# Performance work log

Hardware: AMD Instinct MI355X
Metric: run time of the kernel (lower is better)

Reference implementation:

```python
import jax, jax.numpy as jnp
import numpy as np
import math

C = 512          # in_planes
H = 8            # num_heads
D = C // H       # head_dim = 64
EPS = 1e-12      # torch F.normalize eps


def _l2norm(x):
    # F.normalize(x, dim=-1): x / max(||x||_2, eps)
    n = jnp.sqrt(jnp.sum(x * x, axis=-1, keepdims=True))
    return x / jnp.maximum(n, EPS)


def setup_inputs() -> dict:
    key = jax.random.key(0)
    ks = jax.random.split(key, 8)
    q = jax.random.normal(ks[0], (8, 8, 256, C), dtype=jnp.float32)
    kv = jax.random.normal(ks[1], (8, 8, 512, C), dtype=jnp.float32)
    s = 0.02
    Wq = jax.random.normal(ks[2], (C, C), dtype=jnp.float32) * s
    bq = jax.random.normal(ks[3], (C,), dtype=jnp.float32) * s
    Wkv = jax.random.normal(ks[4], (2 * C, C), dtype=jnp.float32) * s
    bkv = jax.random.normal(ks[5], (2 * C,), dtype=jnp.float32) * s
    Wm = jax.random.normal(ks[6], (C, C), dtype=jnp.float32) * s
    bm = jax.random.normal(ks[7], (C,), dtype=jnp.float32) * s
    return {"q": q, "kv": kv, "Wq": Wq, "bq": bq, "Wkv": Wkv, "bkv": bkv, "Wm": Wm, "bm": bm}


def reference(q, kv, Wq, bq, Wkv, bkv, Wm, bm):
    b, t, lq, c = q.shape
    lk = kv.shape[2]
    shortcut = q

    # Q projection -> (b,t,h,lq,d), L2-normalized over d
    qh = (q @ Wq.T + bq).reshape(b, t, lq, H, D)
    qh = _l2norm(jnp.moveaxis(qh, 3, 2))  # (b,t,h,lq,d)

    # KV projection -> (b,t,2h,lk,d); first H heads = k, last H = v
    kvh = (kv @ Wkv.T + bkv).reshape(b, t, lk, 2 * H, D)
    kvh = jnp.moveaxis(kvh, 3, 2)          # (b,t,2h,lk,d)
    kh = _l2norm(kvh[:, :, :H])            # (b,t,h,lk,d)
    vh = _l2norm(kvh[:, :, H:])            # (b,t,h,lk,d)

    # cosine attention
    att = jnp.einsum('bthqd,bthkd->bthqk', qh, kh) / math.sqrt(D)
    att = jax.nn.softmax(att, axis=-1)
    x = jnp.einsum('bthqk,bthkd->bthqd', att, vh)  # (b,t,h,lq,d)

    # merge heads, output projection, residual
    x = jnp.moveaxis(x, 2, 3).reshape(b, t, lq, c)
    return x @ Wm.T + bm + shortcut
```

## Files before the change

kernel.cpp:

```cpp
#include <hip/hip_runtime.h>
#include <hip/hip_bf16.h>

using bf = __bf16;
typedef __attribute__((ext_vector_type(8))) __bf16 bf16x8;
typedef __attribute__((ext_vector_type(4))) float f32x4;

#define MFMA(a, b, c) __builtin_amdgcn_mfma_f32_16x16x32_bf16((a), (b), (c), 0, 0, 0)
#define GLL16(g, s)                                                         \
    __builtin_amdgcn_global_load_lds(                                       \
        (const __attribute__((address_space(1))) void*)(g),                 \
        (__attribute__((address_space(3))) void*)(s), 16, 0, 0)

__global__ __launch_bounds__(256) void cvt8(const float* __restrict__ s,
                                            bf* __restrict__ d, int n8)
{
    const int i = blockIdx.x * 256 + threadIdx.x;
    if (i >= n8) return;
    const f32x4 a = ((const f32x4*)s)[2 * i];
    const f32x4 b = ((const f32x4*)s)[2 * i + 1];
    bf16x8 r;
#pragma unroll
    for (int k = 0; k < 4; ++k) { r[k] = (bf)a[k]; r[4 + k] = (bf)b[k]; }
    ((bf16x8*)d)[i] = r;
}

template <int EPI>
__global__ __launch_bounds__(256) void gemm128(
    const bf* __restrict__ A, const bf* __restrict__ W,
    const float* __restrict__ bias, const float* __restrict__ res,
    void* __restrict__ Cout, int M, int N, int K)
{
    __shared__ __attribute__((aligned(16))) bf As[128 * 32];
    __shared__ __attribute__((aligned(16))) bf Bs[128 * 32];

    const int lane = threadIdx.x & 63;
    const int wave = threadIdx.x >> 6;
    const int lm = lane & 15;
    const int quad = lane >> 4;
    const int row0 = blockIdx.x * 128, col0 = blockIdx.y * 128;
    const int wrow = (wave >> 1) * 64, wcol = (wave & 1) * 64;

    const int sr = lane >> 2;
    const int sc = (lane & 3) * 8;
    const bf* Ag = A + (size_t)(row0 + wave * 32 + sr) * K + sc;
    const bf* Wg = W + (size_t)(col0 + wave * 32 + sr) * K + sc;
    bf* AsW = As + wave * 1024;
    bf* BsW = Bs + wave * 1024;

    f32x4 acc[4][4] = {};

    for (int k0 = 0; k0 < K; k0 += 32) {
        GLL16(Ag + k0, AsW);
        GLL16(Ag + (size_t)16 * K + k0, AsW + 512);
        GLL16(Wg + k0, BsW);
        GLL16(Wg + (size_t)16 * K + k0, BsW + 512);
        __syncthreads();

        bf16x8 a[4], b[4];
#pragma unroll
        for (int i = 0; i < 4; ++i)
            a[i] = *(const bf16x8*)(As + (wrow + i * 16 + lm) * 32 + quad * 8);
#pragma unroll
        for (int j = 0; j < 4; ++j)
            b[j] = *(const bf16x8*)(Bs + (wcol + j * 16 + lm) * 32 + quad * 8);
#pragma unroll
        for (int i = 0; i < 4; ++i)
#pragma unroll
            for (int j = 0; j < 4; ++j)
                acc[i][j] = MFMA(a[i], b[j], acc[i][j]);
        __syncthreads();
    }

    float bv[4];
#pragma unroll
    for (int j = 0; j < 4; ++j) bv[j] = bias[col0 + wcol + j * 16 + lm];

    if (EPI == 0) {
        bf* C = (bf*)Cout;
#pragma unroll
        for (int i = 0; i < 4; ++i) {
#pragma unroll
            for (int r = 0; r < 4; ++r) {
                float v[4];
                float ss = 0.f;
#pragma unroll
                for (int j = 0; j < 4; ++j) {
                    const float x = acc[i][j][r] + bv[j];
                    v[j] = x;
                    ss += x * x;
                }
                ss += __shfl_xor(ss, 1, 64);
                ss += __shfl_xor(ss, 2, 64);
                ss += __shfl_xor(ss, 4, 64);
                ss += __shfl_xor(ss, 8, 64);
                const float inv = 1.0f / fmaxf(sqrtf(ss), 1e-12f);
                const int row = row0 + wrow + i * 16 + quad * 4 + r;
#pragma unroll
                for (int j = 0; j < 4; ++j)
                    C[(size_t)row * N + col0 + wcol + j * 16 + lm] = (bf)(v[j] * inv);
            }
        }
    } else {
        float* C = (float*)Cout;
#pragma unroll
        for (int i = 0; i < 4; ++i) {
#pragma unroll
            for (int r = 0; r < 4; ++r) {
                const int row = row0 + wrow + i * 16 + quad * 4 + r;
#pragma unroll
                for (int j = 0; j < 4; ++j) {
                    const size_t idx = (size_t)row * N + col0 + wcol + j * 16 + lm;
                    C[idx] = acc[i][j][r] + bv[j] + res[idx];
                }
            }
        }
    }
}

__global__ __launch_bounds__(256) void attn(
    const bf* __restrict__ qn, const bf* __restrict__ kvn, bf* __restrict__ X)
{
    __shared__ __attribute__((aligned(16))) bf kS[512 * 72];
    __shared__ __attribute__((aligned(16))) bf vT[64 * 520];
    __shared__ __attribute__((aligned(16))) bf Ps[4][16 * 40];

    const int bt = blockIdx.x >> 3;
    const int h = blockIdx.x & 7;
    const int tid = threadIdx.x;
    const int lane = tid & 63;
    const int wave = tid >> 6;
    const int lm = lane & 15;
    const int quad = lane >> 4;

    const bf* qh = qn + (size_t)bt * 256 * 512 + h * 64;
    const bf* kh = kvn + (size_t)bt * 512 * 1024 + h * 64;
    const bf* vh = kh + 512;

    {
        const int rr = tid >> 3;
        const int c8 = (tid & 7) * 8;
        for (int it = 0; it < 16; ++it) {
            const int row = it * 32 + rr;
            *(bf16x8*)(&kS[row * 72 + c8]) = *(const bf16x8*)(kh + (size_t)row * 1024 + c8);
        }
        for (int it = 0; it < 16; ++it) {
            const int kk = it * 32 + rr;
            const bf16x8 vv = *(const bf16x8*)(vh + (size_t)kk * 1024 + c8);
#pragma unroll
            for (int j = 0; j < 8; ++j) vT[(c8 + j) * 520 + kk] = vv[j];
        }
    }
    __syncthreads();

    bf* Pw = &Ps[wave][0];

    for (int chunk = 0; chunk < 4; ++chunk) {
        const int r0 = wave * 64 + chunk * 16;

        const bf* qp = qh + (size_t)(r0 + lm) * 512 + quad * 8;
        const bf16x8 a0 = *(const bf16x8*)qp;
        const bf16x8 a1 = *(const bf16x8*)(qp + 32);

        f32x4 s[32];
#pragma unroll
        for (int nt = 0; nt < 32; ++nt) {
            const bf16x8 k0f = *(const bf16x8*)(&kS[(nt * 16 + lm) * 72 + quad * 8]);
            const bf16x8 k1f = *(const bf16x8*)(&kS[(nt * 16 + lm) * 72 + 32 + quad * 8]);
            f32x4 z = {};
            z = MFMA(a0, k0f, z);
            s[nt] = MFMA(a1, k1f, z);
        }

        float mx[4];
#pragma unroll
        for (int rr = 0; rr < 4; ++rr) {
            float m = s[0][rr];
#pragma unroll
            for (int nt = 1; nt < 32; ++nt) m = fmaxf(m, s[nt][rr]);
            m = fmaxf(m, __shfl_xor(m, 1, 64));
            m = fmaxf(m, __shfl_xor(m, 2, 64));
            m = fmaxf(m, __shfl_xor(m, 4, 64));
            m = fmaxf(m, __shfl_xor(m, 8, 64));
            mx[rr] = m;
        }

        f32x4 o[4] = {};
        float sum[4] = {0.f, 0.f, 0.f, 0.f};
        for (int ntp = 0; ntp < 16; ++ntp) {
#pragma unroll
            for (int t = 0; t < 2; ++t) {
#pragma unroll
                for (int rr = 0; rr < 4; ++rr) {
                    const float e = __expf((s[2 * ntp + t][rr] - mx[rr]) * 0.125f);
                    sum[rr] += e;
                    Pw[(quad * 4 + rr) * 40 + t * 16 + lm] = (bf)e;
                }
            }
            const bf16x8 ap = *(const bf16x8*)(&Pw[lm * 40 + quad * 8]);
#pragma unroll
            for (int dt = 0; dt < 4; ++dt) {
                const bf16x8 bv = *(const bf16x8*)(&vT[(dt * 16 + lm) * 520 + ntp * 32 + quad * 8]);
                o[dt] = MFMA(ap, bv, o[dt]);
            }
        }

        float inv_l[4];
#pragma unroll
        for (int rr = 0; rr < 4; ++rr) {
            float sm = sum[rr];
            sm += __shfl_xor(sm, 1, 64);
            sm += __shfl_xor(sm, 2, 64);
            sm += __shfl_xor(sm, 4, 64);
            sm += __shfl_xor(sm, 8, 64);
            inv_l[rr] = 1.0f / sm;
        }

        bf* Xp = X + ((size_t)bt * 256 + r0) * 512 + h * 64;
#pragma unroll
        for (int dt = 0; dt < 4; ++dt)
#pragma unroll
            for (int rr = 0; rr < 4; ++rr)
                Xp[(size_t)(quad * 4 + rr) * 512 + dt * 16 + lm] = (bf)(o[dt][rr] * inv_l[rr]);
    }
}

extern "C" void kernel_launch(void* const* d_in, const int* in_sizes, int n_in,
                              void* d_out, int out_size, void* d_ws, size_t ws_size,
                              hipStream_t stream)
{
    const float* q   = (const float*)d_in[0];
    const float* kv  = (const float*)d_in[1];
    const float* Wq  = (const float*)d_in[2];
    const float* bq  = (const float*)d_in[3];
    const float* Wkv = (const float*)d_in[4];
    const float* bkv = (const float*)d_in[5];
    const float* Wm  = (const float*)d_in[6];
    const float* bm  = (const float*)d_in[7];
    float* out = (float*)d_out;

    char* ws = (char*)d_ws;
    bf* kvb = (bf*)ws;
    bf* kvn = (bf*)(ws + (size_t)(32 << 20));
    bf* wqb = (bf*)ws;
    bf* wmb = (bf*)(ws + (size_t)(16 << 20));
    bf* X   = (bf*)ws;
    char* dob = (char*)d_out;
    bf* wkvb = (bf*)dob;
    bf* qb   = (bf*)dob;
    bf* qn   = (bf*)(dob + (size_t)(16 << 20));

    cvt8<<<dim3(8192), 256, 0, stream>>>(kv, kvb, 2097152);
    cvt8<<<dim3(256), 256, 0, stream>>>(Wkv, wkvb, 65536);
    gemm128<0><<<dim3(256, 8), 256, 0, stream>>>(kvb, wkvb, bkv, nullptr, kvn, 32768, 1024, 512);
    cvt8<<<dim3(4096), 256, 0, stream>>>(q, qb, 1048576);
    cvt8<<<dim3(128), 256, 0, stream>>>(Wq, wqb, 32768);
    cvt8<<<dim3(128), 256, 0, stream>>>(Wm, wmb, 32768);
    gemm128<0><<<dim3(128, 4), 256, 0, stream>>>(qb, wqb, bq, nullptr, qn, 16384, 512, 512);
    attn<<<dim3(512), 256, 0, stream>>>(qn, kvn, X);
    gemm128<1><<<dim3(128, 4), 256, 0, stream>>>(X, wmb, bm, q, out, 16384, 512, 512);
}
```

Measured before the change: 316.6 us.

## Split attention across query blocks with tiled online softmax; merge conversion kernels

The attention kernel now launches four blocks per (batch, head), each covering 64 query rows. It streams K and V through LDS in tiles of 128 keys and uses an online softmax with running max and sum, replacing the previous layout where the whole 512-key K and V sat in LDS. This cuts LDS use sharply and adds occupancy (launch bounds 256,4), at the cost of re-reading K and V from global memory four times per head and adding extra barriers. Separately, the five fp32-to-bf16 conversion launches are merged into two multi-tensor kernels to reduce launch overhead.

Measured after the change: 306.8 us. 3.1% less time.

```diff
diff --git a/kernel.cpp b/kernel.cpp
--- a/kernel.cpp
+++ b/kernel.cpp
@@ -11,17 +11,36 @@
         (const __attribute__((address_space(1))) void*)(g),                 \
         (__attribute__((address_space(3))) void*)(s), 16, 0, 0)
 
-__global__ __launch_bounds__(256) void cvt8(const float* __restrict__ s,
-                                            bf* __restrict__ d, int n8)
-{
-    const int i = blockIdx.x * 256 + threadIdx.x;
-    if (i >= n8) return;
+static __device__ __forceinline__ void cvt_one(const float* __restrict__ s,
+                                               bf* __restrict__ d, int i)
+{
     const f32x4 a = ((const f32x4*)s)[2 * i];
     const f32x4 b = ((const f32x4*)s)[2 * i + 1];
     bf16x8 r;
 #pragma unroll
     for (int k = 0; k < 4; ++k) { r[k] = (bf)a[k]; r[4 + k] = (bf)b[k]; }
     ((bf16x8*)d)[i] = r;
+}
+
+__global__ __launch_bounds__(256) void cvt2(const float* __restrict__ s1, bf* __restrict__ d1, int n1,
+                                            const float* __restrict__ s2, bf* __restrict__ d2, int n2)
+{
+    int i = blockIdx.x * 256 + threadIdx.x;
+    if (i < n1) { cvt_one(s1, d1, i); return; }
+    i -= n1;
+    if (i < n2) cvt_one(s2, d2, i);
+}
+
+__global__ __launch_bounds__(256) void cvt3(const float* __restrict__ s1, bf* __restrict__ d1, int n1,
+                                            const float* __restrict__ s2, bf* __restrict__ d2, int n2,
+                                            const float* __restrict__ s3, bf* __restrict__ d3, int n3)
+{
+    int i = blockIdx.x * 256 + threadIdx.x;
+    if (i < n1) { cvt_one(s1, d1, i); return; }
+    i -= n1;
+    if (i < n2) { cvt_one(s2, d2, i); return; }
+    i -= n2;
+    if (i < n3) cvt_one(s3, d3, i);
 }
 
 template <int EPI>
@@ -117,111 +136,127 @@
     }
 }
 
-__global__ __launch_bounds__(256) void attn(
+__global__ __launch_bounds__(256, 4) void attn(
     const bf* __restrict__ qn, const bf* __restrict__ kvn, bf* __restrict__ X)
 {
-    __shared__ __attribute__((aligned(16))) bf kS[512 * 72];
-    __shared__ __attribute__((aligned(16))) bf vT[64 * 520];
+    __shared__ __attribute__((aligned(16))) bf Kt[128 * 72];
+    __shared__ __attribute__((aligned(16))) bf Vt[64 * 136];
     __shared__ __attribute__((aligned(16))) bf Ps[4][16 * 40];
 
-    const int bt = blockIdx.x >> 3;
-    const int h = blockIdx.x & 7;
+    const int qb = blockIdx.x >> 9;
+    const int rb = blockIdx.x & 511;
+    const int bt = rb >> 3;
+    const int h = rb & 7;
     const int tid = threadIdx.x;
     const int lane = tid & 63;
     const int wave = tid >> 6;
     const int lm = lane & 15;
     const int quad = lane >> 4;
 
-    const bf* qh = qn + (size_t)bt * 256 * 512 + h * 64;
+    const bf* qh = qn + ((size_t)bt * 256 + qb * 64) * 512 + h * 64;
     const bf* kh = kvn + (size_t)bt * 512 * 1024 + h * 64;
     const bf* vh = kh + 512;
 
-    {
-        const int rr = tid >> 3;
-        const int c8 = (tid & 7) * 8;
-        for (int it = 0; it < 16; ++it) {
-            const int row = it * 32 + rr;
-            *(bf16x8*)(&kS[row * 72 + c8]) = *(const bf16x8*)(kh + (size_t)row * 1024 + c8);
-        }
-        for (int it = 0; it < 16; ++it) {
-            const int kk = it * 32 + rr;
-            const bf16x8 vv = *(const bf16x8*)(vh + (size_t)kk * 1024 + c8);
-#pragma unroll
-            for (int j = 0; j < 8; ++j) vT[(c8 + j) * 520 + kk] = vv[j];
-        }
-    }
-    __syncthreads();
-
-    bf* Pw = &Ps[wave][0];
-
-    for (int chunk = 0; chunk < 4; ++chunk) {
-        const int r0 = wave * 64 + chunk * 16;
-
-        const bf* qp = qh + (size_t)(r0 + lm) * 512 + quad * 8;
-        const bf16x8 a0 = *(const bf16x8*)qp;
-        const bf16x8 a1 = *(const bf16x8*)(qp + 32);
-
-        f32x4 s[32];
-#pragma unroll
-        for (int nt = 0; nt < 32; ++nt) {
-            const bf16x8 k0f = *(const bf16x8*)(&kS[(nt * 16 + lm) * 72 + quad * 8]);
-            const bf16x8 k1f = *(const bf16x8*)(&kS[(nt * 16 + lm) * 72 + 32 + quad * 8]);
+    const bf* qp = qh + (size_t)(wave * 16 + lm) * 512 + quad * 8;
+    const bf16x8 a0 = *(const bf16x8*)qp;
+    const bf16x8 a1 = *(const bf16x8*)(qp + 32);
+
+    f32x4 o[4] = {};
+    float mrow[4] = {-1e30f, -1e30f, -1e30f, -1e30f};
+    float lrow[4] = {};
+
+    const int srow = tid >> 1;
+    const int sseg = (tid & 1) * 32;
+
+    for (int t = 0; t < 4; ++t) {
+        {
+            const bf* kr = kh + (size_t)(t * 128 + srow) * 1024 + sseg;
+            bf* kd = Kt + srow * 72 + sseg;
+#pragma unroll
+            for (int j = 0; j < 4; ++j)
+                *(bf16x8*)(kd + j * 8) = *(const bf16x8*)(kr + j * 8);
+
+            const bf* vr = vh + (size_t)(t * 128 + srow) * 1024 + sseg;
+            bf16x8 vv[4];
+#pragma unroll
+            for (int j = 0; j < 4; ++j) vv[j] = *(const bf16x8*)(vr + j * 8);
+#pragma unroll
+            for (int j = 0; j < 4; ++j)
+#pragma unroll
+                for (int e = 0; e < 8; ++e)
+                    Vt[(sseg + j * 8 + e) * 136 + srow] = vv[j][e];
+        }
+        __syncthreads();
+
+        f32x4 s[8];
+#pragma unroll
+        for (int nt = 0; nt < 8; ++nt) {
+            const bf16x8 k0 = *(const bf16x8*)(&Kt[(nt * 16 + lm) * 72 + quad * 8]);
+            const bf16x8 k1 = *(const bf16x8*)(&Kt[(nt * 16 + lm) * 72 + 32 + quad * 8]);
             f32x4 z = {};
-            z = MFMA(a0, k0f, z);
-            s[nt] = MFMA(a1, k1f, z);
-        }
-
-        float mx[4];
+            z = MFMA(a0, k0, z);
+            s[nt] = MFMA(a1, k1, z);
+        }
+
+        float alpha[4], mnew[4];
 #pragma unroll
         for (int rr = 0; rr < 4; ++rr) {
             float m = s[0][rr];
 #pragma unroll
-            for (int nt = 1; nt < 32; ++nt) m = fmaxf(m, s[nt][rr]);
+            for (int nt = 1; nt < 8; ++nt) m = fmaxf(m, s[nt][rr]);
             m = fmaxf(m, __shfl_xor(m, 1, 64));
             m = fmaxf(m, __shfl_xor(m, 2, 64));
             m = fmaxf(m, __shfl_xor(m, 4, 64));
             m = fmaxf(m, __shfl_xor(m, 8, 64));
-            mx[rr] = m;
-        }
-
-        f32x4 o[4] = {};
-        float sum[4] = {0.f, 0.f, 0.f, 0.f};
-        for (int ntp = 0; ntp < 16; ++ntp) {
-#pragma unroll
-            for (int t = 0; t < 2; ++t) {
+            const float mn = fmaxf(mrow[rr], m);
+            alpha[rr] = __expf((mrow[rr] - mn) * 0.125f);
+            mnew[rr] = mn;
+            mrow[rr] = mn;
+        }
+#pragma unroll
+        for (int dt = 0; dt < 4; ++dt)
+#pragma unroll
+            for (int rr = 0; rr < 4; ++rr) o[dt][rr] *= alpha[rr];
+
+        float tsum[4] = {};
+        bf* Pw = &Ps[wave][0];
+        for (int ntp = 0; ntp < 4; ++ntp) {
+#pragma unroll
+            for (int tt = 0; tt < 2; ++tt)
 #pragma unroll
                 for (int rr = 0; rr < 4; ++rr) {
-                    const float e = __expf((s[2 * ntp + t][rr] - mx[rr]) * 0.125f);
-                    sum[rr] += e;
-                    Pw[(quad * 4 + rr) * 40 + t * 16 + lm] = (bf)e;
+                    const float e = __expf((s[ntp * 2 + tt][rr] - mnew[rr]) * 0.125f);
+                    tsum[rr] += e;
+                    Pw[(quad * 4 + rr) * 40 + tt * 16 + lm] = (bf)e;
                 }
-            }
             const bf16x8 ap = *(const bf16x8*)(&Pw[lm * 40 + quad * 8]);
 #pragma unroll
             for (int dt = 0; dt < 4; ++dt) {
-                const bf16x8 bv = *(const bf16x8*)(&vT[(dt * 16 + lm) * 520 + ntp * 32 + quad * 8]);
+                const bf16x8 bv = *(const bf16x8*)(&Vt[(dt * 16 + lm) * 136 + ntp * 32 + quad * 8]);
                 o[dt] = MFMA(ap, bv, o[dt]);
             }
         }
-
-        float inv_l[4];
 #pragma unroll
         for (int rr = 0; rr < 4; ++rr) {
-            float sm = sum[rr];
+            float sm = tsum[rr];
             sm += __shfl_xor(sm, 1, 64);
             sm += __shfl_xor(sm, 2, 64);
             sm += __shfl_xor(sm, 4, 64);
             sm += __shfl_xor(sm, 8, 64);
-            inv_l[rr] = 1.0f / sm;
-        }
-
-        bf* Xp = X + ((size_t)bt * 256 + r0) * 512 + h * 64;
-#pragma unroll
-        for (int dt = 0; dt < 4; ++dt)
-#pragma unroll
-            for (int rr = 0; rr < 4; ++rr)
-                Xp[(size_t)(quad * 4 + rr) * 512 + dt * 16 + lm] = (bf)(o[dt][rr] * inv_l[rr]);
+            lrow[rr] = lrow[rr] * alpha[rr] + sm;
+        }
+        __syncthreads();
     }
+
+    float inv[4];
+#pragma unroll
+    for (int rr = 0; rr < 4; ++rr) inv[rr] = 1.0f / lrow[rr];
+    bf* Xp = X + ((size_t)bt * 256 + qb * 64 + wave * 16) * 512 + h * 64;
+#pragma unroll
+    for (int dt = 0; dt < 4; ++dt)
+#pragma unroll
+        for (int rr = 0; rr < 4; ++rr)
+            Xp[(size_t)(quad * 4 + rr) * 512 + dt * 16 + lm] = (bf)(o[dt][rr] * inv[rr]);
 }
 
 extern "C" void kernel_launch(void* const* d_in, const int* in_sizes, int n_in,
@@ -249,13 +284,10 @@
     bf* qb   = (bf*)dob;
     bf* qn   = (bf*)(dob + (size_t)(16 << 20));
 
-    cvt8<<<dim3(8192), 256, 0, stream>>>(kv, kvb, 2097152);
-    cvt8<<<dim3(256), 256, 0, stream>>>(Wkv, wkvb, 65536);
+    cvt2<<<dim3(8448), 256, 0, stream>>>(kv, kvb, 2097152, Wkv, wkvb, 65536);
     gemm128<0><<<dim3(256, 8), 256, 0, stream>>>(kvb, wkvb, bkv, nullptr, kvn, 32768, 1024, 512);
-    cvt8<<<dim3(4096), 256, 0, stream>>>(q, qb, 1048576);
-    cvt8<<<dim3(128), 256, 0, stream>>>(Wq, wqb, 32768);
-    cvt8<<<dim3(128), 256, 0, stream>>>(Wm, wmb, 32768);
+    cvt3<<<dim3(4352), 256, 0, stream>>>(q, qb, 1048576, Wq, wqb, 32768, Wm, wmb, 32768);
     gemm128<0><<<dim3(128, 4), 256, 0, stream>>>(qb, wqb, bq, nullptr, qn, 16384, 512, 512);
-    attn<<<dim3(512), 256, 0, stream>>>(qn, kvn, X);
+    attn<<<dim3(2048), 256, 0, stream>>>(qn, kvn, X);
     gemm128<1><<<dim3(128, 4), 256, 0, stream>>>(X, wmb, bm, q, out, 16384, 512, 512);
 }
```
